# Kernel optimization log

Hardware: AMD Instinct MI355X
Metric: run time of the kernel (lower is better)

The kernel has to match this reference:

```python
import jax, jax.numpy as jnp
import numpy as np

HEADS = 8
DIM_HEAD = 32
IH = IW = 32
EPS = 1e-5


def _relative_index(ih, iw):
    # faithful reproduction of the torch buffer computation
    coords = np.stack(np.meshgrid(np.arange(ih), np.arange(iw), indexing='ij')).reshape(2, -1)  # (2, n)
    rel = coords[:, :, None] - coords[:, None, :]  # (2, n, n)
    rel[0] += ih - 1
    rel[1] += iw - 1
    rel[0] *= 2 * iw - 1
    return rel.transpose(1, 2, 0).sum(-1).reshape(-1).astype(np.int32)  # (n*n,)


def setup_inputs() -> dict:
    key = jax.random.key(0)
    ks = jax.random.split(key, 8)
    C, HID = 256, 1024
    s = 0.02
    inp = {
        'x': jax.random.normal(ks[0], (16, C, IH, IW), jnp.float32),
        'qkv_w': jax.random.normal(ks[1], (C, 3 * HEADS * DIM_HEAD), jnp.float32) * s,
        'proj_w': jax.random.normal(ks[2], (HEADS * DIM_HEAD, C), jnp.float32) * s,
        'proj_b': jnp.zeros((C,), jnp.float32),
        'ffn_w1': jax.random.normal(ks[3], (C, HID), jnp.float32) * s,
        'ffn_b1': jnp.zeros((HID,), jnp.float32),
        'ffn_w2': jax.random.normal(ks[4], (HID, C), jnp.float32) * s,
        'ffn_b2': jnp.zeros((C,), jnp.float32),
        'norm1_w': jnp.ones((C,), jnp.float32),
        'norm1_b': jnp.zeros((C,), jnp.float32),
        'norm2_w': jnp.ones((C,), jnp.float32),
        'norm2_b': jnp.zeros((C,), jnp.float32),
        'bias_table': jax.random.normal(ks[5], ((2 * IH - 1) * (2 * IW - 1), HEADS), jnp.float32) * s,
        'rel_index': jnp.asarray(_relative_index(IH, IW)),
    }
    return inp


def _layernorm(x, w, b):
    mu = jnp.mean(x, -1, keepdims=True)
    var = jnp.mean(jnp.square(x - mu), -1, keepdims=True)
    return (x - mu) * jax.lax.rsqrt(var + EPS) * w + b


def reference(x, qkv_w, proj_w, proj_b, ffn_w1, ffn_b1, ffn_w2, ffn_b2,
              norm1_w, norm1_b, norm2_w, norm2_b, bias_table, rel_index):
    B, C, H, W = x.shape
    n = H * W
    scale = DIM_HEAD ** -0.5

    # b c h w -> b n c
    xt = x.reshape(B, C, n).transpose(0, 2, 1)
    x1 = _layernorm(xt, norm1_w, norm1_b)

    qkv = x1 @ qkv_w  # (B, n, 3*inner)
    q, k, v = jnp.split(qkv, 3, axis=-1)
    def heads(t):
        return t.reshape(B, n, HEADS, DIM_HEAD).transpose(0, 2, 1, 3)  # b h n d
    q, k, v = heads(q), heads(k), heads(v)

    dots = jnp.einsum('bhid,bhjd->bhij', q, k) * scale
    # gathered relative position bias: (n*n, heads) -> (1, heads, n, n)
    bias = bias_table[rel_index].reshape(n, n, HEADS).transpose(2, 0, 1)[None]
    attn = jax.nn.softmax(dots + bias, axis=-1)
    out = jnp.einsum('bhij,bhjd->bhid', attn, v)  # b h n d
    out = out.transpose(0, 2, 1, 3).reshape(B, n, HEADS * DIM_HEAD)
    out = out @ proj_w + proj_b  # (B, n, C)

    # back to b c h w and first residual
    x1 = out.transpose(0, 2, 1).reshape(B, C, H, W)
    x3 = x1 + x

    # FFN branch
    x4 = x3.reshape(B, C, n).transpose(0, 2, 1)
    x4 = _layernorm(x4, norm2_w, norm2_b)
    x4 = jax.nn.gelu(x4 @ ffn_w1 + ffn_b1, approximate=False) @ ffn_w2 + ffn_b2
    x4 = x4.transpose(0, 2, 1).reshape(B, C, H, W)
    return x3 + x4
```

## Files before the change

kernel.cpp:

```cpp
#include <hip/hip_runtime.h>
#include <math.h>

#define BATCH 16
#define CH    256
#define NT    1024
#define NH    8
#define DH    32
#define HID   1024
#define MROWS (BATCH * NT)
#define LN_EPS 1e-5f

typedef unsigned short u16;
typedef unsigned int u32;
typedef __attribute__((ext_vector_type(8))) short short8;
typedef __attribute__((ext_vector_type(4))) short short4v;
typedef __attribute__((ext_vector_type(4))) float f32x4;

struct __align__(8) US4 { u16 x, y, z, w; };
struct __align__(16) F4 { float x, y, z, w; };

#define MFMA(a, b, c) __builtin_amdgcn_mfma_f32_16x16x32_bf16((a), (b), (c), 0, 0, 0)
#define MFMA16(a, b, c) __builtin_amdgcn_mfma_f32_16x16x16bf16_1k((a), (b), (c), 0, 0, 0)

#define LOG2E 1.4426950408889634f
#define QSCALE (0.17677669529663687f * 1.4426950408889634f)

__device__ __forceinline__ float bf2f(u16 u) {
  union { unsigned int i; float f; } v; v.i = ((unsigned int)u) << 16; return v.f;
}
__device__ __forceinline__ u16 f2bf(float f) {
  union { float f; unsigned int i; } v; v.f = f;
  unsigned int i = v.i;
  return (u16)((i + 0x7fffu + ((i >> 16) & 1u)) >> 16);
}
__device__ __forceinline__ u32 pack_bf16_pair(float lo, float hi) {
  union { float f; u32 i; } a, b; a.f = lo; b.f = hi;
#if defined(__HIP_DEVICE_COMPILE__)
  return __builtin_amdgcn_perm(b.i, a.i, 0x07060302u);
#else
  return (b.i & 0xFFFF0000u) | (a.i >> 16);
#endif
}
__device__ __forceinline__ float fast_exp2(float x) {
#if defined(__HIP_DEVICE_COMPILE__)
  return __builtin_amdgcn_exp2f(x);
#else
  return exp2f(x);
#endif
}
__device__ __forceinline__ float fast_gelu(float x) {
  const float c = 2.0f * LOG2E * 0.7978845608028654f;
  float t = fast_exp2(c * (x + 0.044715f * x * x * x));
  return x * t / (t + 1.0f);
}
__device__ __forceinline__ void llds16(const u16* g, u16* l) {
  __builtin_amdgcn_global_load_lds(
      (const __attribute__((address_space(1))) u32*)g,
      (__attribute__((address_space(3))) u32*)l, 16, 0, 0);
}

__global__ __launch_bounds__(256) void k_transpose(const float* __restrict__ in,
                                                   u16* __restrict__ out,
                                                   int K, int N) {
  __shared__ u16 tl[64][66];
  const int t = threadIdx.x;
  const int kb = blockIdx.x * 64, nb = blockIdx.y * 64;
#pragma unroll
  for (int it = 0; it < 16; ++it) {
    int n_l = t & 63, k_l = it * 4 + (t >> 6);
    tl[k_l][n_l] = f2bf(in[(size_t)(kb + k_l) * N + nb + n_l]);
  }
  __syncthreads();
#pragma unroll
  for (int it = 0; it < 16; ++it) {
    int k_l = t & 63, n_l = it * 4 + (t >> 6);
    out[(size_t)(nb + n_l) * K + kb + k_l] = tl[k_l][n_l];
  }
}

__global__ __launch_bounds__(256) void k_prep_bias(const float* __restrict__ table,
                                                   const int* __restrict__ rel,
                                                   u16* __restrict__ biasL) {
  const int t = threadIdx.x;
  const int jt = blockIdx.x & 31, isl = blockIdx.x >> 5;
  const int jp = t & 31, io = t >> 5;
  for (int ib = isl * 128; ib < isl * 128 + 128; ib += 8) {
    int i = ib + io;
    int idx = rel[(size_t)i * NT + jt * 32 + jp];
#pragma unroll
    for (int h = 0; h < NH; ++h) {
      biasL[(((size_t)h * 32 + jt) * 1024 + i) * 32 + jp] =
          f2bf(table[(size_t)idx * NH + h] * LOG2E);
    }
  }
}

__global__ __launch_bounds__(256) void k_ln1(const float* __restrict__ x,
                                             const float* __restrict__ w,
                                             const float* __restrict__ b,
                                             u16* __restrict__ x1) {
  __shared__ u16 tile[CH][68];
  __shared__ float red_s[4][64], red_q[4][64], mu_s[64], rs_s[64];
  const int t = threadIdx.x;
  const int bb = blockIdx.x >> 4, pb = blockIdx.x & 15;
  const int pos0 = pb * 64;
#pragma unroll
  for (int it = 0; it < 16; ++it) {
    int c = it * 16 + (t >> 4), p4 = (t & 15) * 4;
    F4 v = *(const F4*)(x + ((size_t)bb * CH + c) * NT + pos0 + p4);
    US4 o; o.x = f2bf(v.x); o.y = f2bf(v.y); o.z = f2bf(v.z); o.w = f2bf(v.w);
    *(US4*)&tile[c][p4] = o;
  }
  __syncthreads();
  {
    int pos = t & 63, g = t >> 6;
    float s = 0.f, q = 0.f;
#pragma unroll 8
    for (int cc = 0; cc < 64; ++cc) {
      float v = bf2f(tile[g * 64 + cc][pos]);
      s += v; q += v * v;
    }
    red_s[g][pos] = s; red_q[g][pos] = q;
  }
  __syncthreads();
  if (t < 64) {
    float s = red_s[0][t] + red_s[1][t] + red_s[2][t] + red_s[3][t];
    float q = red_q[0][t] + red_q[1][t] + red_q[2][t] + red_q[3][t];
    float mu = s * (1.f / CH);
    float var = q * (1.f / CH) - mu * mu;
    mu_s[t] = mu;
    rs_s[t] = rsqrtf(fmaxf(var, 0.f) + LN_EPS);
  }
  __syncthreads();
  {
    const int c = t;
    const float wv = w[c], bv = b[c];
    for (int pos = 0; pos < 64; ++pos) {
      float v = (bf2f(tile[c][pos]) - mu_s[pos]) * rs_s[pos] * wv + bv;
      x1[((size_t)bb * NT + pos0 + pos) * CH + c] = f2bf(v);
    }
  }
}

template <int K>
__device__ __forceinline__ void gemm128(const u16* __restrict__ A,
                                        const u16* __restrict__ Bt,
                                        int r0, int c0, int tid,
                                        u16* lA, u16* lB,
                                        f32x4 acc[4][4]) {
  const int wave = tid >> 6, lane = tid & 63;
  const int wm = (wave >> 1) * 64, wn = (wave & 1) * 64;
  const int l16 = lane & 15, quad = lane >> 4;
  const int srow = lane >> 2;
  const int scol = (lane & 3) * 8;
  const u16* gA0 = A + (size_t)(r0 + wave * 16 + srow) * K + scol;
  const u16* gA1 = A + (size_t)(r0 + wave * 16 + 64 + srow) * K + scol;
  const u16* gB0 = Bt + (size_t)(c0 + wave * 16 + srow) * K + scol;
  const u16* gB1 = Bt + (size_t)(c0 + wave * 16 + 64 + srow) * K + scol;
  u16* lA0 = lA + (wave * 16) * 32;
  u16* lA1 = lA + (wave * 16 + 64) * 32;
  u16* lB0 = lB + (wave * 16) * 32;
  u16* lB1 = lB + (wave * 16 + 64) * 32;
  for (int k0 = 0; k0 < K; k0 += 32) {
    __syncthreads();
    llds16(gA0 + k0, lA0);
    llds16(gA1 + k0, lA1);
    llds16(gB0 + k0, lB0);
    llds16(gB1 + k0, lB1);
    __syncthreads();
    short8 af[4], bf[4];
#pragma unroll
    for (int i = 0; i < 4; ++i)
      af[i] = *(const short8*)&lA[(wm + i * 16 + l16) * 32 + quad * 8];
#pragma unroll
    for (int j = 0; j < 4; ++j)
      bf[j] = *(const short8*)&lB[(wn + j * 16 + l16) * 32 + quad * 8];
#pragma unroll
    for (int i = 0; i < 4; ++i)
#pragma unroll
      for (int j = 0; j < 4; ++j)
        acc[i][j] = MFMA(af[i], bf[j], acc[i][j]);
  }
}

#define GEMM_PROLOGUE(KVAL, APTR, BPTR)                                  \
  __shared__ __align__(16) u16 lA[128 * 32];                             \
  __shared__ __align__(16) u16 lB[128 * 32];                             \
  const int tid = threadIdx.x;                                           \
  const int wave = tid >> 6, lane = tid & 63;                            \
  const int wm = (wave >> 1) * 64, wn = (wave & 1) * 64;                 \
  const int l16 = lane & 15, quad = lane >> 4;                           \
  const int r0 = blockIdx.x * 128, c0 = blockIdx.y * 128;                \
  f32x4 acc[4][4];                                                       \
  _Pragma("unroll") for (int i = 0; i < 4; ++i)                          \
  _Pragma("unroll") for (int j = 0; j < 4; ++j) acc[i][j] = 0.f;         \
  gemm128<KVAL>(APTR, BPTR, r0, c0, tid, lA, lB, acc);

__global__ __launch_bounds__(256) void k_gemm_qkv(const u16* __restrict__ x1,
                                                  const u16* __restrict__ wT,
                                                  u16* __restrict__ q,
                                                  u16* __restrict__ k,
                                                  u16* __restrict__ vT) {
  GEMM_PROLOGUE(CH, x1, wT)
#pragma unroll
  for (int j = 0; j < 4; ++j) {
    int col = c0 + wn + j * 16 + l16;
    int which = col >> 8, rem = col & 255, h = rem >> 5, dd = rem & 31;
#pragma unroll
    for (int i = 0; i < 4; ++i) {
      int row0 = r0 + wm + i * 16 + quad * 4;
      int bb = row0 >> 10, pos = row0 & 1023;
      if (which == 2) {
        US4 o;
        o.x = f2bf(acc[i][j][0]); o.y = f2bf(acc[i][j][1]);
        o.z = f2bf(acc[i][j][2]); o.w = f2bf(acc[i][j][3]);
        *(US4*)(vT + (((size_t)bb * NH + h) * DH + dd) * NT + pos) = o;
      } else {
        u16* dst = (which == 0) ? q : k;
        float mul = (which == 0) ? QSCALE : 1.0f;
#pragma unroll
        for (int r = 0; r < 4; ++r)
          dst[(((size_t)bb * NH + h) * NT + pos + r) * DH + dd] =
              f2bf(acc[i][j][r] * mul);
      }
    }
  }
}

__global__ __launch_bounds__(256) void k_gemm_proj(const u16* __restrict__ ao,
                                                   const u16* __restrict__ wT,
                                                   const float* __restrict__ pb,
                                                   const float* __restrict__ x,
                                                   u16* __restrict__ x3) {
  GEMM_PROLOGUE(CH, ao, wT)
#pragma unroll
  for (int j = 0; j < 4; ++j) {
    int col = c0 + wn + j * 16 + l16;
    float bias = pb[col];
#pragma unroll
    for (int i = 0; i < 4; ++i) {
      int row0 = r0 + wm + i * 16 + quad * 4;
      int bb = row0 >> 10, pos = row0 & 1023;
#pragma unroll
      for (int r = 0; r < 4; ++r) {
        float val = acc[i][j][r] + bias + x[((size_t)bb * CH + col) * NT + pos + r];
        x3[(size_t)(row0 + r) * CH + col] = f2bf(val);
      }
    }
  }
}

__global__ __launch_bounds__(256) void k_gemm_ffn1(const u16* __restrict__ a,
                                                   const u16* __restrict__ wT,
                                                   const float* __restrict__ b1,
                                                   u16* __restrict__ hmat) {
  GEMM_PROLOGUE(CH, a, wT)
#pragma unroll
  for (int j = 0; j < 4; ++j) {
    int col = c0 + wn + j * 16 + l16;
    float bias = b1[col];
#pragma unroll
    for (int i = 0; i < 4; ++i) {
      int row0 = r0 + wm + i * 16 + quad * 4;
#pragma unroll
      for (int r = 0; r < 4; ++r) {
        float v = acc[i][j][r] + bias;
        hmat[(size_t)(row0 + r) * HID + col] = f2bf(fast_gelu(v));
      }
    }
  }
}

__global__ __launch_bounds__(256) void k_gemm_ffn2(const u16* __restrict__ a,
                                                   const u16* __restrict__ wT,
                                                   const float* __restrict__ b2,
                                                   u16* __restrict__ x4) {
  GEMM_PROLOGUE(HID, a, wT)
#pragma unroll
  for (int j = 0; j < 4; ++j) {
    int col = c0 + wn + j * 16 + l16;
    float bias = b2[col];
#pragma unroll
    for (int i = 0; i < 4; ++i) {
      int row0 = r0 + wm + i * 16 + quad * 4;
#pragma unroll
      for (int r = 0; r < 4; ++r)
        x4[(size_t)(row0 + r) * CH + col] = f2bf(acc[i][j][r] + bias);
    }
  }
}

__global__ __launch_bounds__(256) void k_attn(const u16* __restrict__ q,
                                              const u16* __restrict__ k,
                                              const u16* __restrict__ vT,
                                              const u16* __restrict__ biasL,
                                              u16* __restrict__ ao) {
  __shared__ u16 Ks[256][40];
  __shared__ u16 Vt[32][264];
  const int tid = threadIdx.x;
  const int wave = tid >> 6, lane = tid & 63;
  const int quad = lane >> 4, l16 = lane & 15;
  const int bh = blockIdx.x >> 4, qt = blockIdx.x & 15;
  const int h = bh & 7, bb = bh >> 3;
  const int i0 = qt * 64 + wave * 16;

  short8 aq = *(const short8*)(q + ((size_t)bh * NT + i0 + l16) * DH + quad * 8);
  const u16* bias_base =
      biasL + (((size_t)h * 32) * 1024 + (i0 + l16)) * 32 + quad * 4;

  float l_loc = 0.f;
  f32x4 accd0 = 0.f, accd1 = 0.f;

  for (int chunk = 0; chunk < 4; ++chunk) {
    __syncthreads();
    const int rbase = chunk * 256;
    {
      const int srow = tid >> 3, sdd = (tid & 7) * 4;
#pragma unroll
      for (int it = 0; it < 8; ++it) {
        int rl = it * 32 + srow;
        US4 kv = *(const US4*)(k + ((size_t)bh * NT + rbase + rl) * DH + sdd);
        *(US4*)&Ks[rl][sdd] = kv;
      }
      const int j4 = (tid & 63) * 4;
#pragma unroll
      for (int it = 0; it < 8; ++it) {
        int d = it * 4 + wave;
        US4 vv = *(const US4*)(vT + ((size_t)bh * DH + d) * NT + rbase + j4);
        *(US4*)&Vt[d][j4] = vv;
      }
    }
    __syncthreads();

#pragma unroll 2
    for (int j0 = 0; j0 < 256; j0 += 32) {
      const int jt = (rbase + j0) >> 5;
      const u16* bl = bias_base + (size_t)jt * 32768;
      US4 b0 = *(const US4*)bl;
      US4 b1 = *(const US4*)(bl + 16);
      f32x4 cc0, cc1;
      cc0[0] = bf2f(b0.x); cc0[1] = bf2f(b0.y);
      cc0[2] = bf2f(b0.z); cc0[3] = bf2f(b0.w);
      cc1[0] = bf2f(b1.x); cc1[1] = bf2f(b1.y);
      cc1[2] = bf2f(b1.z); cc1[3] = bf2f(b1.w);
      short8 ak0 = *(const short8*)&Ks[j0 + l16][quad * 8];
      short8 ak1 = *(const short8*)&Ks[j0 + 16 + l16][quad * 8];
      f32x4 s0 = MFMA(ak0, aq, cc0);
      f32x4 s1 = MFMA(ak1, aq, cc1);
      float p00 = fast_exp2(s0[0]), p01 = fast_exp2(s0[1]);
      float p02 = fast_exp2(s0[2]), p03 = fast_exp2(s0[3]);
      float p10 = fast_exp2(s1[0]), p11 = fast_exp2(s1[1]);
      float p12 = fast_exp2(s1[2]), p13 = fast_exp2(s1[3]);
      l_loc += ((p00 + p01) + (p02 + p03)) + ((p10 + p11) + (p12 + p13));
      union { u32 u[2]; short4v s; } pa0, pa1;
      pa0.u[0] = pack_bf16_pair(p00, p01);
      pa0.u[1] = pack_bf16_pair(p02, p03);
      pa1.u[0] = pack_bf16_pair(p10, p11);
      pa1.u[1] = pack_bf16_pair(p12, p13);
      short4v vb00 = *(const short4v*)&Vt[l16][j0 + quad * 4];
      short4v vb10 = *(const short4v*)&Vt[l16][j0 + 16 + quad * 4];
      short4v vb01 = *(const short4v*)&Vt[16 + l16][j0 + quad * 4];
      short4v vb11 = *(const short4v*)&Vt[16 + l16][j0 + 16 + quad * 4];
      accd0 = MFMA16(pa0.s, vb00, accd0);
      accd1 = MFMA16(pa0.s, vb01, accd1);
      accd0 = MFMA16(pa1.s, vb10, accd0);
      accd1 = MFMA16(pa1.s, vb11, accd1);
    }
  }
  l_loc += __shfl_xor(l_loc, 16);
  l_loc += __shfl_xor(l_loc, 32);
#pragma unroll
  for (int r = 0; r < 4; ++r) {
    float lr = __shfl(l_loc, quad * 4 + r);
    float inv = 1.0f / lr;
    int row = i0 + quad * 4 + r;
    u16* o = ao + ((size_t)bb * NT + row) * CH + h * DH;
    o[l16]      = f2bf(accd0[r] * inv);
    o[16 + l16] = f2bf(accd1[r] * inv);
  }
}

__global__ __launch_bounds__(256) void k_ln2(const u16* __restrict__ x3,
                                             const float* __restrict__ w,
                                             const float* __restrict__ b,
                                             u16* __restrict__ x4ln) {
  const int wave = threadIdx.x >> 6, lane = threadIdx.x & 63;
  const size_t row = (size_t)blockIdx.x * 4 + wave;
  US4 u = *(const US4*)(x3 + row * CH + lane * 4);
  float v0 = bf2f(u.x), v1 = bf2f(u.y), v2 = bf2f(u.z), v3 = bf2f(u.w);
  float s = v0 + v1 + v2 + v3;
  float qq = v0 * v0 + v1 * v1 + v2 * v2 + v3 * v3;
#pragma unroll
  for (int mask = 1; mask <= 32; mask <<= 1) {
    s += __shfl_xor(s, mask);
    qq += __shfl_xor(qq, mask);
  }
  float mu = s * (1.f / CH);
  float var = qq * (1.f / CH) - mu * mu;
  float rs = rsqrtf(fmaxf(var, 0.f) + LN_EPS);
  F4 uw = *(const F4*)(w + lane * 4);
  F4 ub = *(const F4*)(b + lane * 4);
  US4 o;
  o.x = f2bf((v0 - mu) * rs * uw.x + ub.x);
  o.y = f2bf((v1 - mu) * rs * uw.y + ub.y);
  o.z = f2bf((v2 - mu) * rs * uw.z + ub.z);
  o.w = f2bf((v3 - mu) * rs * uw.w + ub.w);
  *(US4*)(x4ln + row * CH + lane * 4) = o;
}

__global__ __launch_bounds__(256) void k_add_t(const u16* __restrict__ x3,
                                               const u16* __restrict__ x4,
                                               float* __restrict__ out) {
  __shared__ float tl[64][66];
  const int t = threadIdx.x;
  const int bb = blockIdx.x >> 6;
  const int pb = (blockIdx.x >> 2) & 15, cb = blockIdx.x & 3;
  const int pos0 = pb * 64, c0 = cb * 64;
#pragma unroll
  for (int it = 0; it < 16; ++it) {
    int c_l = t & 63, p_l = it * 4 + (t >> 6);
    size_t ro = ((size_t)bb * NT + pos0 + p_l) * CH + c0 + c_l;
    tl[p_l][c_l] = bf2f(x3[ro]) + bf2f(x4[ro]);
  }
  __syncthreads();
#pragma unroll
  for (int it = 0; it < 16; ++it) {
    int p_l = t & 63, c_l = it * 4 + (t >> 6);
    out[((size_t)bb * CH + c0 + c_l) * NT + pos0 + p_l] = tl[p_l][c_l];
  }
}

extern "C" void kernel_launch(void* const* d_in, const int* in_sizes, int n_in,
                              void* d_out, int out_size, void* d_ws, size_t ws_size,
                              hipStream_t stream) {
  const float* x       = (const float*)d_in[0];
  const float* qkv_w   = (const float*)d_in[1];
  const float* proj_w  = (const float*)d_in[2];
  const float* proj_b  = (const float*)d_in[3];
  const float* ffn_w1  = (const float*)d_in[4];
  const float* ffn_b1  = (const float*)d_in[5];
  const float* ffn_w2  = (const float*)d_in[6];
  const float* ffn_b2  = (const float*)d_in[7];
  const float* norm1_w = (const float*)d_in[8];
  const float* norm1_b = (const float*)d_in[9];
  const float* norm2_w = (const float*)d_in[10];
  const float* norm2_b = (const float*)d_in[11];
  const float* btab    = (const float*)d_in[12];
  const int* rel       = (const int*)d_in[13];
  float* out = (float*)d_out;

  char* ws = (char*)d_ws;
  size_t off = 0;
  auto alloc = [&](size_t bytes) { char* p = ws + off; off += bytes; return p; };
  u16* qkv_wT  = (u16*)alloc((size_t)768 * 256 * 2);
  u16* proj_wT = (u16*)alloc((size_t)256 * 256 * 2);
  u16* w1T     = (u16*)alloc((size_t)1024 * 256 * 2);
  u16* w2T     = (u16*)alloc((size_t)256 * 1024 * 2);
  u16* biasL   = (u16*)alloc((size_t)NH * NT * NT * 2);
  u16* qm      = (u16*)alloc((size_t)MROWS * CH * 2);
  u16* km      = (u16*)alloc((size_t)MROWS * CH * 2);
  u16* vm      = (u16*)alloc((size_t)MROWS * CH * 2);
  u16* bufX    = (u16*)alloc((size_t)MROWS * CH * 2);
  u16* x3      = (u16*)alloc((size_t)MROWS * CH * 2);
  u16* ffn_h = biasL;
  u16* x4ln  = vm;
  u16* x1 = bufX;
  u16* ao = bufX;
  u16* x4 = bufX;
  (void)ws_size; (void)in_sizes; (void)n_in; (void)out_size;

  k_transpose<<<dim3(4, 12), 256, 0, stream>>>(qkv_w, qkv_wT, 256, 768);
  k_transpose<<<dim3(4, 4), 256, 0, stream>>>(proj_w, proj_wT, 256, 256);
  k_transpose<<<dim3(4, 16), 256, 0, stream>>>(ffn_w1, w1T, 256, 1024);
  k_transpose<<<dim3(16, 4), 256, 0, stream>>>(ffn_w2, w2T, 1024, 256);
  k_prep_bias<<<256, 256, 0, stream>>>(btab, rel, biasL);
  k_ln1<<<BATCH * 16, 256, 0, stream>>>(x, norm1_w, norm1_b, x1);
  k_gemm_qkv<<<dim3(MROWS / 128, 6), 256, 0, stream>>>(x1, qkv_wT, qm, km, vm);
  k_attn<<<BATCH * NH * 16, 256, 0, stream>>>(qm, km, vm, biasL, ao);
  k_gemm_proj<<<dim3(MROWS / 128, 2), 256, 0, stream>>>(ao, proj_wT, proj_b, x, x3);
  k_ln2<<<MROWS / 4, 256, 0, stream>>>(x3, norm2_w, norm2_b, x4ln);
  k_gemm_ffn1<<<dim3(MROWS / 128, 8), 256, 0, stream>>>(x4ln, w1T, ffn_b1, ffn_h);
  k_gemm_ffn2<<<dim3(MROWS / 128, 2), 256, 0, stream>>>(ffn_h, w2T, ffn_b2, x4);
  k_add_t<<<BATCH * 16 * 4, 256, 0, stream>>>(x3, x4, out);
}
```

Before: 253.8 us.

## Fuse residual add and transpose into FFN2 epilogue; double query rows per attention block

The FFN2 GEMM epilogue now adds the x3 residual and writes fp32 output directly in the channel-major layout, removing the separate add/transpose kernel and the bf16 round-trip through x4. The attention kernel now handles two 16-row query groups per wave, so each block covers 128 queries and the K/V tiles staged in shared memory are reused twice, halving the block count. The trade-offs are more registers per thread in attention and strided output stores in FFN2.

```diff
diff --git a/kernel.cpp b/kernel.cpp
--- a/kernel.cpp
+++ b/kernel.cpp
@@ -274,18 +274,23 @@
 __global__ __launch_bounds__(256) void k_gemm_ffn2(const u16* __restrict__ a,
                                                    const u16* __restrict__ wT,
                                                    const float* __restrict__ b2,
-                                                   u16* __restrict__ x4) {
+                                                   const u16* __restrict__ x3,
+                                                   float* __restrict__ out) {
   GEMM_PROLOGUE(HID, a, wT)
 #pragma unroll
   for (int j = 0; j < 4; ++j) {
     int col = c0 + wn + j * 16 + l16;
-    float bias = b2[col];
+    float bias = b2[j * 16 + l16 + c0 + wn];
 #pragma unroll
     for (int i = 0; i < 4; ++i) {
       int row0 = r0 + wm + i * 16 + quad * 4;
+      int bb = row0 >> 10, pos = row0 & 1023;
+      F4 o;
+      float* po = &o.x;
 #pragma unroll
       for (int r = 0; r < 4; ++r)
-        x4[(size_t)(row0 + r) * CH + col] = f2bf(acc[i][j][r] + bias);
+        po[r] = acc[i][j][r] + bias + bf2f(x3[(size_t)(row0 + r) * CH + col]);
+      *(F4*)(out + ((size_t)bb * CH + col) * NT + pos) = o;
     }
   }
 }
@@ -300,16 +305,21 @@
   const int tid = threadIdx.x;
   const int wave = tid >> 6, lane = tid & 63;
   const int quad = lane >> 4, l16 = lane & 15;
-  const int bh = blockIdx.x >> 4, qt = blockIdx.x & 15;
+  const int bh = blockIdx.x >> 3, qt = blockIdx.x & 7;
   const int h = bh & 7, bb = bh >> 3;
-  const int i0 = qt * 64 + wave * 16;
-
-  short8 aq = *(const short8*)(q + ((size_t)bh * NT + i0 + l16) * DH + quad * 8);
-  const u16* bias_base =
-      biasL + (((size_t)h * 32) * 1024 + (i0 + l16)) * 32 + quad * 4;
-
-  float l_loc = 0.f;
-  f32x4 accd0 = 0.f, accd1 = 0.f;
+  const int i0 = qt * 128 + wave * 16;
+
+  short8 aq[2];
+  const u16* bias_base[2];
+  float l_loc[2] = {0.f, 0.f};
+  f32x4 accd0[2], accd1[2];
+#pragma unroll
+  for (int g = 0; g < 2; ++g) {
+    aq[g] = *(const short8*)(q + ((size_t)bh * NT + i0 + g * 64 + l16) * DH + quad * 8);
+    bias_base[g] =
+        biasL + (((size_t)h * 32) * 1024 + (i0 + g * 64 + l16)) * 32 + quad * 4;
+    accd0[g] = 0.f; accd1[g] = 0.f;
+  }
 
   for (int chunk = 0; chunk < 4; ++chunk) {
     __syncthreads();
@@ -332,51 +342,58 @@
     }
     __syncthreads();
 
-#pragma unroll 2
+#pragma unroll
     for (int j0 = 0; j0 < 256; j0 += 32) {
       const int jt = (rbase + j0) >> 5;
-      const u16* bl = bias_base + (size_t)jt * 32768;
-      US4 b0 = *(const US4*)bl;
-      US4 b1 = *(const US4*)(bl + 16);
-      f32x4 cc0, cc1;
-      cc0[0] = bf2f(b0.x); cc0[1] = bf2f(b0.y);
-      cc0[2] = bf2f(b0.z); cc0[3] = bf2f(b0.w);
-      cc1[0] = bf2f(b1.x); cc1[1] = bf2f(b1.y);
-      cc1[2] = bf2f(b1.z); cc1[3] = bf2f(b1.w);
       short8 ak0 = *(const short8*)&Ks[j0 + l16][quad * 8];
       short8 ak1 = *(const short8*)&Ks[j0 + 16 + l16][quad * 8];
-      f32x4 s0 = MFMA(ak0, aq, cc0);
-      f32x4 s1 = MFMA(ak1, aq, cc1);
-      float p00 = fast_exp2(s0[0]), p01 = fast_exp2(s0[1]);
-      float p02 = fast_exp2(s0[2]), p03 = fast_exp2(s0[3]);
-      float p10 = fast_exp2(s1[0]), p11 = fast_exp2(s1[1]);
-      float p12 = fast_exp2(s1[2]), p13 = fast_exp2(s1[3]);
-      l_loc += ((p00 + p01) + (p02 + p03)) + ((p10 + p11) + (p12 + p13));
-      union { u32 u[2]; short4v s; } pa0, pa1;
-      pa0.u[0] = pack_bf16_pair(p00, p01);
-      pa0.u[1] = pack_bf16_pair(p02, p03);
-      pa1.u[0] = pack_bf16_pair(p10, p11);
-      pa1.u[1] = pack_bf16_pair(p12, p13);
       short4v vb00 = *(const short4v*)&Vt[l16][j0 + quad * 4];
       short4v vb10 = *(const short4v*)&Vt[l16][j0 + 16 + quad * 4];
       short4v vb01 = *(const short4v*)&Vt[16 + l16][j0 + quad * 4];
       short4v vb11 = *(const short4v*)&Vt[16 + l16][j0 + 16 + quad * 4];
-      accd0 = MFMA16(pa0.s, vb00, accd0);
-      accd1 = MFMA16(pa0.s, vb01, accd1);
-      accd0 = MFMA16(pa1.s, vb10, accd0);
-      accd1 = MFMA16(pa1.s, vb11, accd1);
-    }
-  }
-  l_loc += __shfl_xor(l_loc, 16);
-  l_loc += __shfl_xor(l_loc, 32);
-#pragma unroll
-  for (int r = 0; r < 4; ++r) {
-    float lr = __shfl(l_loc, quad * 4 + r);
-    float inv = 1.0f / lr;
-    int row = i0 + quad * 4 + r;
-    u16* o = ao + ((size_t)bb * NT + row) * CH + h * DH;
-    o[l16]      = f2bf(accd0[r] * inv);
-    o[16 + l16] = f2bf(accd1[r] * inv);
+#pragma unroll
+      for (int g = 0; g < 2; ++g) {
+        const u16* bl = bias_base[g] + (size_t)jt * 32768;
+        US4 b0 = *(const US4*)bl;
+        US4 b1 = *(const US4*)(bl + 16);
+        f32x4 cc0, cc1;
+        cc0[0] = bf2f(b0.x); cc0[1] = bf2f(b0.y);
+        cc0[2] = bf2f(b0.z); cc0[3] = bf2f(b0.w);
+        cc1[0] = bf2f(b1.x); cc1[1] = bf2f(b1.y);
+        cc1[2] = bf2f(b1.z); cc1[3] = bf2f(b1.w);
+        f32x4 s0 = MFMA(ak0, aq[g], cc0);
+        f32x4 s1 = MFMA(ak1, aq[g], cc1);
+        float p00 = fast_exp2(s0[0]), p01 = fast_exp2(s0[1]);
+        float p02 = fast_exp2(s0[2]), p03 = fast_exp2(s0[3]);
+        float p10 = fast_exp2(s1[0]), p11 = fast_exp2(s1[1]);
+        float p12 = fast_exp2(s1[2]), p13 = fast_exp2(s1[3]);
+        l_loc[g] += ((p00 + p01) + (p02 + p03)) + ((p10 + p11) + (p12 + p13));
+        union { u32 u[2]; short4v s; } pa0, pa1;
+        pa0.u[0] = pack_bf16_pair(p00, p01);
+        pa0.u[1] = pack_bf16_pair(p02, p03);
+        pa1.u[0] = pack_bf16_pair(p10, p11);
+        pa1.u[1] = pack_bf16_pair(p12, p13);
+        accd0[g] = MFMA16(pa0.s, vb00, accd0[g]);
+        accd1[g] = MFMA16(pa0.s, vb01, accd1[g]);
+        accd0[g] = MFMA16(pa1.s, vb10, accd0[g]);
+        accd1[g] = MFMA16(pa1.s, vb11, accd1[g]);
+      }
+    }
+  }
+#pragma unroll
+  for (int g = 0; g < 2; ++g) {
+    float ll = l_loc[g];
+    ll += __shfl_xor(ll, 16);
+    ll += __shfl_xor(ll, 32);
+#pragma unroll
+    for (int r = 0; r < 4; ++r) {
+      float lr = __shfl(ll, quad * 4 + r);
+      float inv = 1.0f / lr;
+      int row = i0 + g * 64 + quad * 4 + r;
+      u16* o = ao + ((size_t)bb * NT + row) * CH + h * DH;
+      o[l16]      = f2bf(accd0[g][r] * inv);
+      o[16 + l16] = f2bf(accd1[g][r] * inv);
+    }
   }
 }
 
@@ -406,28 +423,6 @@
   o.z = f2bf((v2 - mu) * rs * uw.z + ub.z);
   o.w = f2bf((v3 - mu) * rs * uw.w + ub.w);
   *(US4*)(x4ln + row * CH + lane * 4) = o;
-}
-
-__global__ __launch_bounds__(256) void k_add_t(const u16* __restrict__ x3,
-                                               const u16* __restrict__ x4,
-                                               float* __restrict__ out) {
-  __shared__ float tl[64][66];
-  const int t = threadIdx.x;
-  const int bb = blockIdx.x >> 6;
-  const int pb = (blockIdx.x >> 2) & 15, cb = blockIdx.x & 3;
-  const int pos0 = pb * 64, c0 = cb * 64;
-#pragma unroll
-  for (int it = 0; it < 16; ++it) {
-    int c_l = t & 63, p_l = it * 4 + (t >> 6);
-    size_t ro = ((size_t)bb * NT + pos0 + p_l) * CH + c0 + c_l;
-    tl[p_l][c_l] = bf2f(x3[ro]) + bf2f(x4[ro]);
-  }
-  __syncthreads();
-#pragma unroll
-  for (int it = 0; it < 16; ++it) {
-    int p_l = t & 63, c_l = it * 4 + (t >> 6);
-    out[((size_t)bb * CH + c0 + c_l) * NT + pos0 + p_l] = tl[p_l][c_l];
-  }
 }
 
 extern "C" void kernel_launch(void* const* d_in, const int* in_sizes, int n_in,
@@ -466,7 +461,6 @@
   u16* x4ln  = vm;
   u16* x1 = bufX;
   u16* ao = bufX;
-  u16* x4 = bufX;
   (void)ws_size; (void)in_sizes; (void)n_in; (void)out_size;
 
   k_transpose<<<dim3(4, 12), 256, 0, stream>>>(qkv_w, qkv_wT, 256, 768);
@@ -476,10 +470,9 @@
   k_prep_bias<<<256, 256, 0, stream>>>(btab, rel, biasL);
   k_ln1<<<BATCH * 16, 256, 0, stream>>>(x, norm1_w, norm1_b, x1);
   k_gemm_qkv<<<dim3(MROWS / 128, 6), 256, 0, stream>>>(x1, qkv_wT, qm, km, vm);
-  k_attn<<<BATCH * NH * 16, 256, 0, stream>>>(qm, km, vm, biasL, ao);
+  k_attn<<<BATCH * NH * 8, 256, 0, stream>>>(qm, km, vm, biasL, ao);
   k_gemm_proj<<<dim3(MROWS / 128, 2), 256, 0, stream>>>(ao, proj_wT, proj_b, x, x3);
   k_ln2<<<MROWS / 4, 256, 0, stream>>>(x3, norm2_w, norm2_b, x4ln);
   k_gemm_ffn1<<<dim3(MROWS / 128, 8), 256, 0, stream>>>(x4ln, w1T, ffn_b1, ffn_h);
-  k_gemm_ffn2<<<dim3(MROWS / 128, 2), 256, 0, stream>>>(ffn_h, w2T, ffn_b2, x4);
-  k_add_t<<<BATCH * 16 * 4, 256, 0, stream>>>(x3, x4, out);
-}
+  k_gemm_ffn2<<<dim3(MROWS / 128, 2), 256, 0, stream>>>(ffn_h, w2T, ffn_b2, x3, out);
+}
```

New measurement: 255.9 us. No clear change (+0.8%).
